# Optimization experiments

Hardware: AMD Instinct MI355X
Metric: run time of the kernel (lower is better)

## Reference

```python
import jax, jax.numpy as jnp
import numpy as np

B, L, H = 256, 512, 256      # batch, seq_len, hid_dim
REL_VOCAB = 50000            # relation_input_dim
A = 100000                   # size of global action pool (len(actions))
K = 512                      # action keys per sample (padded ragged dim)
ENT_VOCAB = 40000
PAD = 0                      # entity_pad_idx


def setup_inputs() -> dict:
    key = jax.random.key(0)
    k1, k2, k3, k4, k5, k6 = jax.random.split(key, 6)
    entities = jax.random.randint(k1, (B, L), 0, ENT_VOCAB)
    relations = jax.random.randint(k2, (B, L), 0, REL_VOCAB)
    actions = jax.random.randint(k3, (A,), 0, REL_VOCAB)
    action_keys = jax.random.randint(k4, (B, K), 0, A)
    encoded = jax.random.normal(k5, (B, L, H), dtype=jnp.float32)  # opaque encoder output
    rel_emb = jax.random.normal(k6, (REL_VOCAB, H), dtype=jnp.float32) * 0.02
    return {"entities": entities, "relations": relations, "actions": actions,
            "action_keys": action_keys, "encoded": encoded, "rel_emb": rel_emb}


def reference(entities, relations, actions, action_keys, encoded, rel_emb):
    # mask-based gather of the last non-pad position per sample
    mask = (entities != PAD)                       # [B, L]
    idxs = mask.sum(axis=1) - 1                    # [B]
    enc_last = jnp.take_along_axis(
        encoded, idxs[:, None, None], axis=1).squeeze(1)  # [B, H]
    # only_relations branch: action embedding lookup for the global action pool
    action_emb = rel_emb[actions]                  # [A, H]
    # ragged (padded) per-sample gather + matvec: preds[b,k] = action_emb[keys[b,k]] . enc_last[b]
    gathered = action_emb[action_keys]             # [B, K, H]
    preds = jnp.einsum('bkh,bh->bk', gathered, enc_last)  # [B, K]
    return preds
```

## Files before the change

### kernel.cpp

```cpp
#include <hip/hip_runtime.h>

#define B 256
#define L 512
#define H 256
#define K 512
#define CHUNKS 4
#define KPB (K / CHUNKS)
#define THREADS 256

__global__ __launch_bounds__(THREADS)
void preds_fused_kernel(const int* __restrict__ entities,
                        const int* __restrict__ actions,
                        const int* __restrict__ action_keys,
                        const float* __restrict__ encoded,
                        const float* __restrict__ rel_emb,
                        float* __restrict__ out)
{
    const int blk   = blockIdx.x;
    const int b     = blk >> 2;
    const int chunk = blk & 3;
    const int t     = threadIdx.x;
    const int lane  = t & 63;
    const int wave  = t >> 6;

    __shared__ int s_count;
    if (t == 0) s_count = 0;
    __syncthreads();

    int c = (entities[b * L + t] != 0) + (entities[b * L + t + 256] != 0);
    #pragma unroll
    for (int off = 32; off > 0; off >>= 1)
        c += __shfl_down(c, off, 64);
    if (lane == 0) atomicAdd(&s_count, c);
    __syncthreads();

    int idx = s_count - 1;
    idx = max(0, min(L - 1, idx));

    const float4 e =
        *(const float4*)&encoded[((size_t)(b * L + idx)) * H + lane * 4];

    const int  kbase = chunk * KPB + wave * (KPB / 4);
    const int* ak    = action_keys + b * K;

    #pragma unroll 2
    for (int i = 0; i < KPB / 4; i += 4) {
        const int k0 = kbase + i;
        int a0 = actions[ak[k0 + 0]];
        int a1 = actions[ak[k0 + 1]];
        int a2 = actions[ak[k0 + 2]];
        int a3 = actions[ak[k0 + 3]];

        float4 r0 = *(const float4*)&rel_emb[(size_t)a0 * H + lane * 4];
        float4 r1 = *(const float4*)&rel_emb[(size_t)a1 * H + lane * 4];
        float4 r2 = *(const float4*)&rel_emb[(size_t)a2 * H + lane * 4];
        float4 r3 = *(const float4*)&rel_emb[(size_t)a3 * H + lane * 4];

        float p0 = r0.x * e.x + r0.y * e.y + r0.z * e.z + r0.w * e.w;
        float p1 = r1.x * e.x + r1.y * e.y + r1.z * e.z + r1.w * e.w;
        float p2 = r2.x * e.x + r2.y * e.y + r2.z * e.z + r2.w * e.w;
        float p3 = r3.x * e.x + r3.y * e.y + r3.z * e.z + r3.w * e.w;

        #pragma unroll
        for (int off = 1; off < 64; off <<= 1) {
            p0 += __shfl_xor(p0, off, 64);
            p1 += __shfl_xor(p1, off, 64);
            p2 += __shfl_xor(p2, off, 64);
            p3 += __shfl_xor(p3, off, 64);
        }
        if (lane == 0) {
            out[b * K + k0 + 0] = p0;
            out[b * K + k0 + 1] = p1;
            out[b * K + k0 + 2] = p2;
            out[b * K + k0 + 3] = p3;
        }
    }
}

extern "C" void kernel_launch(void* const* d_in, const int* in_sizes, int n_in,
                              void* d_out, int out_size, void* d_ws, size_t ws_size,
                              hipStream_t stream)
{
    const int*   entities    = (const int*)d_in[0];
    const int*   actions     = (const int*)d_in[2];
    const int*   action_keys = (const int*)d_in[3];
    const float* encoded     = (const float*)d_in[4];
    const float* rel_emb     = (const float*)d_in[5];
    float*       out         = (float*)d_out;

    hipLaunchKernelGGL(preds_fused_kernel,
                       dim3(B * CHUNKS), dim3(THREADS), 0, stream,
                       entities, actions, action_keys, encoded, rel_emb, out);
}
```

Before: 26.00 us.

## Split waves into 16-lane groups per key with preloaded action indices

Each wave is now divided into four 16-lane groups, and each group computes the dot product for its own key, so the cross-lane reduction takes 4 shuffle steps instead of 6 and produces four results per step. The per-wave action indices are loaded once, one per lane, and broadcast with shuffles, replacing serial dependent index loads inside the loop. The mask count uses ballot and popcount, and the grid doubles to 8 chunks per sample to raise occupancy. In exchange each lane keeps more float4 registers live.

```diff
diff --git a/kernel.cpp b/kernel.cpp
--- a/kernel.cpp
+++ b/kernel.cpp
@@ -4,9 +4,11 @@
 #define L 512
 #define H 256
 #define K 512
-#define CHUNKS 4
+#define CHUNKS 8
 #define KPB (K / CHUNKS)
 #define THREADS 256
+#define KPW (KPB / 4)
+#define KPG (KPW / 4)
 
 __global__ __launch_bounds__(THREADS)
 void preds_fused_kernel(const int* __restrict__ entities,
@@ -17,62 +19,76 @@
                         float* __restrict__ out)
 {
     const int blk   = blockIdx.x;
-    const int b     = blk >> 2;
-    const int chunk = blk & 3;
+    const int b     = blk >> 3;
+    const int chunk = blk & 7;
     const int t     = threadIdx.x;
     const int lane  = t & 63;
     const int wave  = t >> 6;
+    const int gid   = lane >> 4;
+    const int gl    = lane & 15;
 
     __shared__ int s_count;
     if (t == 0) s_count = 0;
     __syncthreads();
 
-    int c = (entities[b * L + t] != 0) + (entities[b * L + t + 256] != 0);
-    #pragma unroll
-    for (int off = 32; off > 0; off >>= 1)
-        c += __shfl_down(c, off, 64);
-    if (lane == 0) atomicAdd(&s_count, c);
+    {
+        unsigned long long m0 = __ballot(entities[b * L + t] != 0);
+        unsigned long long m1 = __ballot(entities[b * L + t + 256] != 0);
+        if (lane == 0) atomicAdd(&s_count, __popcll(m0) + __popcll(m1));
+    }
     __syncthreads();
 
     int idx = s_count - 1;
     idx = max(0, min(L - 1, idx));
 
-    const float4 e =
-        *(const float4*)&encoded[((size_t)(b * L + idx)) * H + lane * 4];
+    const int kw = chunk * KPB + wave * KPW;
+    const int* ak = action_keys + b * K;
+    int av = 0;
+    if (lane < KPW) av = actions[ak[kw + lane]];
 
-    const int  kbase = chunk * KPB + wave * (KPB / 4);
-    const int* ak    = action_keys + b * K;
+    const float* encrow = &encoded[((size_t)(b * L + idx)) * H];
+    const float4 e0 = *(const float4*)&encrow[gl * 4];
+    const float4 e1 = *(const float4*)&encrow[gl * 4 + 64];
+    const float4 e2 = *(const float4*)&encrow[gl * 4 + 128];
+    const float4 e3 = *(const float4*)&encrow[gl * 4 + 192];
 
-    #pragma unroll 2
-    for (int i = 0; i < KPB / 4; i += 4) {
-        const int k0 = kbase + i;
-        int a0 = actions[ak[k0 + 0]];
-        int a1 = actions[ak[k0 + 1]];
-        int a2 = actions[ak[k0 + 2]];
-        int a3 = actions[ak[k0 + 3]];
+    #pragma unroll
+    for (int i = 0; i < KPG; i += 2) {
+        const int o0 = gid * KPG + i;
+        const int o1 = o0 + 1;
+        const int a0 = __shfl(av, o0, 64);
+        const int a1 = __shfl(av, o1, 64);
 
-        float4 r0 = *(const float4*)&rel_emb[(size_t)a0 * H + lane * 4];
-        float4 r1 = *(const float4*)&rel_emb[(size_t)a1 * H + lane * 4];
-        float4 r2 = *(const float4*)&rel_emb[(size_t)a2 * H + lane * 4];
-        float4 r3 = *(const float4*)&rel_emb[(size_t)a3 * H + lane * 4];
+        const float* r0 = &rel_emb[(size_t)a0 * H];
+        const float* r1 = &rel_emb[(size_t)a1 * H];
 
-        float p0 = r0.x * e.x + r0.y * e.y + r0.z * e.z + r0.w * e.w;
-        float p1 = r1.x * e.x + r1.y * e.y + r1.z * e.z + r1.w * e.w;
-        float p2 = r2.x * e.x + r2.y * e.y + r2.z * e.z + r2.w * e.w;
-        float p3 = r3.x * e.x + r3.y * e.y + r3.z * e.z + r3.w * e.w;
+        float4 r00 = *(const float4*)&r0[gl * 4];
+        float4 r01 = *(const float4*)&r0[gl * 4 + 64];
+        float4 r02 = *(const float4*)&r0[gl * 4 + 128];
+        float4 r03 = *(const float4*)&r0[gl * 4 + 192];
+        float4 r10 = *(const float4*)&r1[gl * 4];
+        float4 r11 = *(const float4*)&r1[gl * 4 + 64];
+        float4 r12 = *(const float4*)&r1[gl * 4 + 128];
+        float4 r13 = *(const float4*)&r1[gl * 4 + 192];
+
+        float p0 = r00.x * e0.x + r00.y * e0.y + r00.z * e0.z + r00.w * e0.w;
+        p0 += r01.x * e1.x + r01.y * e1.y + r01.z * e1.z + r01.w * e1.w;
+        p0 += r02.x * e2.x + r02.y * e2.y + r02.z * e2.z + r02.w * e2.w;
+        p0 += r03.x * e3.x + r03.y * e3.y + r03.z * e3.z + r03.w * e3.w;
+
+        float p1 = r10.x * e0.x + r10.y * e0.y + r10.z * e0.z + r10.w * e0.w;
+        p1 += r11.x * e1.x + r11.y * e1.y + r11.z * e1.z + r11.w * e1.w;
+        p1 += r12.x * e2.x + r12.y * e2.y + r12.z * e2.z + r12.w * e2.w;
+        p1 += r13.x * e3.x + r13.y * e3.y + r13.z * e3.z + r13.w * e3.w;
 
         #pragma unroll
-        for (int off = 1; off < 64; off <<= 1) {
+        for (int off = 1; off < 16; off <<= 1) {
             p0 += __shfl_xor(p0, off, 64);
             p1 += __shfl_xor(p1, off, 64);
-            p2 += __shfl_xor(p2, off, 64);
-            p3 += __shfl_xor(p3, off, 64);
         }
-        if (lane == 0) {
-            out[b * K + k0 + 0] = p0;
-            out[b * K + k0 + 1] = p1;
-            out[b * K + k0 + 2] = p2;
-            out[b * K + k0 + 3] = p3;
+        if (gl == 0) {
+            out[b * K + kw + o0] = p0;
+            out[b * K + kw + o1] = p1;
         }
     }
 }
```

Result: faster. 25.05 us (-3.7%).
